# Kernel optimization log

Measured on AMD Instinct MI355X. Metric: run time of the kernel, lower is better.

## Reference

```python
import jax, jax.numpy as jnp
import numpy as np

BLOCK = 512
WINDOW = 2
NEG = -1e9


def _pad_to_block(x, block):
    pad_len = (-x.shape[1]) % block
    if pad_len:
        x = jnp.pad(x, ((0, 0), (0, pad_len), (0, 0)))
    return x


def setup_inputs() -> dict:
    key = jax.random.key(0)
    ks = jax.random.split(key, 8)
    B, Lq, Lk, C = 2, 8192, 8192, 128
    s = 1.0 / np.sqrt(C)
    return {
        "query": jax.random.normal(ks[0], (B, Lq, C), jnp.float32),
        "key_value": jax.random.normal(ks[1], (B, Lk, C), jnp.float32),
        "Wq": jax.random.normal(ks[2], (C, C), jnp.float32) * s,
        "bq": jax.random.normal(ks[3], (C,), jnp.float32) * 0.01,
        "Wkv": jax.random.normal(ks[4], (C, 2 * C), jnp.float32) * s,
        "bkv": jax.random.normal(ks[5], (2 * C,), jnp.float32) * 0.01,
        "Wo": jax.random.normal(ks[6], (C, C), jnp.float32) * s,
        "bo": jax.random.normal(ks[7], (C,), jnp.float32) * 0.01,
    }


def reference(query, key_value, Wq, bq, Wkv, bkv, Wo, bo):
    B, Lq, C = query.shape
    qp = _pad_to_block(query, BLOCK)
    kp = _pad_to_block(key_value, BLOCK)
    q = qp @ Wq + bq                      # [B, Lq_pad, C]
    kv = kp @ Wkv + bkv                   # [B, Lk_pad, 2C]
    k, v = kv[..., :C], kv[..., C:]
    nq = qp.shape[1] // BLOCK
    nk = kp.shape[1] // BLOCK
    qb = q.reshape(B, nq, BLOCK, C)
    kb = k.reshape(B, nk, BLOCK, C)
    vb = v.reshape(B, nk, BLOCK, C)
    allowed = jnp.abs(jnp.arange(nq)[:, None] - jnp.arange(nk)[None, :]) <= WINDOW  # [nq, nk]
    # scores: [B, nq, nk, s, d] with s = q-pos in block, d = k-pos in block
    scores = jnp.einsum('bqsc,bkdc->bqksd', qb, kb) / jnp.sqrt(jnp.asarray(C, qb.dtype))
    scores = jnp.where(allowed[None, :, :, None, None], scores, NEG)
    # NOTE: faithful to original torch code, softmax over axis=3 (the 's' axis)
    attn = jax.nn.softmax(scores, axis=3)
    out = jnp.einsum('bqksd,bkdc->bqsc', attn, vb)
    out = out.reshape(B, nq * BLOCK, C)[:, :Lq]
    return out @ Wo + bo
```

## Files before the change

### kernel.cpp

```cpp
#include <hip/hip_runtime.h>

typedef _Float16 f16;
typedef _Float16 half8 __attribute__((ext_vector_type(8)));
typedef float floatx4 __attribute__((ext_vector_type(4)));

#define MFMA16(a,b,c) __builtin_amdgcn_mfma_f32_16x16x32_f16((a),(b),(c),0,0,0)
#define RSL2E 0.12751743f

__device__ __forceinline__ void split2(float x, f16 &h, f16 &l) {
  f16 hh = (f16)x;
  h = hh;
  l = (f16)(x - (float)hh);
}

__device__ __forceinline__ void stage_rows64(const f16* __restrict__ g, int gstride,
                                             f16* lds, int rows, int tid, int nthr) {
  int total = rows * 8;
  for (int idx = tid; idx < total; idx += nthr) {
    int row = idx >> 3, slot = idx & 7;
    float4 v = *(const float4*)(g + (size_t)row * gstride + slot * 8);
    int lofs = ((row << 7) + (slot << 4)) ^ ((row & 7) << 4);
    *(float4*)((char*)lds + lofs) = v;
  }
}
__device__ __forceinline__ void stage_rows128(const f16* __restrict__ g, int gstride,
                                              f16* lds, int rows, int tid, int nthr) {
  int total = rows * 16;
  for (int idx = tid; idx < total; idx += nthr) {
    int row = idx >> 4, slot = idx & 15;
    float4 v = *(const float4*)(g + (size_t)row * gstride + slot * 8);
    int lofs = ((row << 8) + (slot << 4)) ^ ((row & 7) << 4);
    *(float4*)((char*)lds + lofs) = v;
  }
}
__device__ __forceinline__ void stage_split64(const float* __restrict__ g, int gstride,
                                              f16* ldsh, f16* ldsl, int rows,
                                              int tid, int nthr) {
  int total = rows * 16;
  for (int idx = tid; idx < total; idx += nthr) {
    int row = idx >> 4, cg = idx & 15;
    float4 va = *(const float4*)(g + (size_t)row * gstride + cg * 4);
    union { f16 a[4]; uint2 u; } hh, ll;
    split2(va.x, hh.a[0], ll.a[0]);
    split2(va.y, hh.a[1], ll.a[1]);
    split2(va.z, hh.a[2], ll.a[2]);
    split2(va.w, hh.a[3], ll.a[3]);
    int lofs = ((row << 7) + (cg << 3)) ^ ((row & 7) << 4);
    *(uint2*)((char*)ldsh + lofs) = hh.u;
    *(uint2*)((char*)ldsl + lofs) = ll.u;
  }
}
__device__ __forceinline__ half8 fragP128(const f16* lds, int row, int kofs) {
  int ofs = ((row << 7) + (kofs << 1)) ^ ((row & 7) << 4);
  return *(const half8*)((const char*)lds + ofs);
}
__device__ __forceinline__ half8 fragP256(const f16* lds, int row, int kofs) {
  int ofs = ((row << 8) + (kofs << 1)) ^ ((row & 7) << 4);
  return *(const half8*)((const char*)lds + ofs);
}

__global__ void k_splitW(const float* __restrict__ Wq, const float* __restrict__ Wkv,
                         const float* __restrict__ Wo,
                         f16* WqTh, f16* WqTl, f16* WkvTh, f16* WkvTl,
                         f16* WoTh, f16* WoTl) {
  int idx = blockIdx.x * 256 + threadIdx.x;
  if (idx >= 65536) return;
  float v; f16 *ph, *pl; int dst;
  if (idx < 16384) {
    int n = idx >> 7, c = idx & 127;
    v = Wq[c * 128 + n]; ph = WqTh; pl = WqTl; dst = idx;
  } else if (idx < 49152) {
    int t = idx - 16384; int n = t >> 7, c = t & 127;
    v = Wkv[c * 256 + n]; ph = WkvTh; pl = WkvTl; dst = t;
  } else {
    int t = idx - 49152; int n = t >> 7, c = t & 127;
    v = Wo[c * 128 + n]; ph = WoTh; pl = WoTl; dst = t;
  }
  f16 h, l; split2(v, h, l);
  ph[dst] = h; pl[dst] = l;
}

__global__ __launch_bounds__(512, 2)
void k_proj(const float* __restrict__ query, const float* __restrict__ key_value,
            const f16* __restrict__ WqTh, const f16* __restrict__ WqTl,
            const f16* __restrict__ WkvTh, const f16* __restrict__ WkvTl,
            const float* __restrict__ bq, const float* __restrict__ bkv,
            f16* __restrict__ qhp, f16* __restrict__ khp, f16* __restrict__ vT) {
  int pidx = blockIdx.x >> 8, blk = blockIdx.x & 255;
  const float* A; const f16 *BTh, *BTl; const float* bias; f16* out; int mode;
  if (pidx == 0)      { A = query;     BTh = WqTh;          BTl = WqTl;          bias = bq;        out = qhp; mode = 0; }
  else if (pidx == 1) { A = key_value; BTh = WkvTh;         BTl = WkvTl;         bias = bkv;       out = khp; mode = 0; }
  else                { A = key_value; BTh = WkvTh + 16384; BTl = WkvTl + 16384; bias = bkv + 128; out = vT;  mode = 1; }
  __shared__ f16 pool[24576];
  f16* sAh = pool;
  f16* sAl = pool + 4096;
  f16* sBh = pool + 8192;
  f16* sBl = pool + 16384;
  int tid = threadIdx.x, wave = tid >> 6, lane = tid & 63, lg = lane >> 4, lr = lane & 15;
  int wm = wave >> 2, wn = wave & 3;
  size_t rowbase = (size_t)blk * 64;
  floatx4 zero = {0.f, 0.f, 0.f, 0.f};
  floatx4 acc[2][2] = {{zero, zero}, {zero, zero}};
  for (int cc = 0; cc < 128; cc += 64) {
    __syncthreads();
    stage_split64(A + rowbase * 128 + cc, 128, sAh, sAl, 64, tid, 512);
    stage_rows64(BTh + cc, 128, sBh, 128, tid, 512);
    stage_rows64(BTl + cc, 128, sBl, 128, tid, 512);
    __syncthreads();
    for (int kc = 0; kc < 64; kc += 32) {
      half8 ah[2], al[2];
      for (int fm = 0; fm < 2; fm++) {
        ah[fm] = fragP128(sAh, wm * 32 + fm * 16 + lr, kc + lg * 8);
        al[fm] = fragP128(sAl, wm * 32 + fm * 16 + lr, kc + lg * 8);
      }
      for (int fn = 0; fn < 2; fn++) {
        half8 bh = fragP128(sBh, wn * 32 + fn * 16 + lr, kc + lg * 8);
        half8 bl = fragP128(sBl, wn * 32 + fn * 16 + lr, kc + lg * 8);
        for (int fm = 0; fm < 2; fm++) {
          acc[fm][fn] = MFMA16(ah[fm], bh, acc[fm][fn]);
          acc[fm][fn] = MFMA16(ah[fm], bl, acc[fm][fn]);
          acc[fm][fn] = MFMA16(al[fm], bh, acc[fm][fn]);
        }
      }
    }
  }
  __syncthreads();
  f16* e = pool;
  for (int fm = 0; fm < 2; fm++) for (int fn = 0; fn < 2; fn++) {
    int n = wn * 32 + fn * 16 + lr;
    float bs = bias[n];
    for (int jj = 0; jj < 4; jj++) {
      int m = wm * 32 + fm * 16 + lg * 4 + jj;
      e[m * 136 + n] = (f16)(acc[fm][fn][jj] + bs);
    }
  }
  __syncthreads();
  if (mode == 0) {
    for (int idx = tid; idx < 1024; idx += 512) {
      int r = idx >> 4, sl = idx & 15;
      *(float4*)(out + (rowbase + r) * 128 + sl * 8) =
          *(const float4*)((const char*)e + r * 272 + sl * 16);
    }
  } else {
    size_t bidx = rowbase >> 13, lofs = rowbase & 8191;
    for (int idx = tid; idx < 1024; idx += 512) {
      int c = idx >> 3, sl = idx & 7;
      union { f16 a[8]; float4 v; } th;
      for (int t = 0; t < 8; t++) th.a[t] = e[(sl * 8 + t) * 136 + c];
      *(float4*)(out + (bidx * 128 + c) * 8192 + lofs + sl * 8) = th.v;
    }
  }
}

__global__ __launch_bounds__(512, 2)
void k_final(const float* __restrict__ Pbuf, const float* __restrict__ U,
             const f16* __restrict__ BTh, const f16* __restrict__ BTl,
             const float* __restrict__ bias, float* __restrict__ out) {
  __shared__ f16 pool[24576];
  f16* sAh = pool;
  f16* sAl = pool + 4096;
  f16* sBh = pool + 8192;
  f16* sBl = pool + 16384;
  int tid = threadIdx.x, wave = tid >> 6, lane = tid & 63, lg = lane >> 4, lr = lane & 15;
  int wm = wave >> 2, wn = wave & 3;
  size_t rowbase = (size_t)blockIdx.x * 64;
  int b = (int)(rowbase >> 13), r0 = (int)(rowbase & 8191);
  int i = r0 >> 9, st = (r0 >> 6) & 7;
  const float* p0 = Pbuf + ((size_t)(((b * 16 + i) * 8 + st) * 4)) * 8192;
  const float* p1 = p0 + 8192;
  const float* p2 = p0 + 16384;
  const float* p3 = p0 + 24576;
  const float* Ub = U + ((size_t)b * 16 + i) * 128;
  floatx4 zero = {0.f, 0.f, 0.f, 0.f};
  floatx4 acc[2][2] = {{zero, zero}, {zero, zero}};
  for (int cc = 0; cc < 128; cc += 64) {
    __syncthreads();
    for (int idx = tid; idx < 1024; idx += 512) {
      int row = idx >> 4, cg = idx & 15;
      int c = cc + cg * 4;
      float4 a0 = *(const float4*)(p0 + row * 128 + c);
      float4 a1 = *(const float4*)(p1 + row * 128 + c);
      float4 a2 = *(const float4*)(p2 + row * 128 + c);
      float4 a3 = *(const float4*)(p3 + row * 128 + c);
      float4 uu = *(const float4*)(Ub + c);
      float vals[4] = {(a0.x + a1.x) + (a2.x + a3.x) + uu.x,
                       (a0.y + a1.y) + (a2.y + a3.y) + uu.y,
                       (a0.z + a1.z) + (a2.z + a3.z) + uu.z,
                       (a0.w + a1.w) + (a2.w + a3.w) + uu.w};
      union { f16 a[4]; uint2 u; } hh, ll;
      for (int t = 0; t < 4; t++) split2(vals[t], hh.a[t], ll.a[t]);
      int lofs = ((row << 7) + (cg << 3)) ^ ((row & 7) << 4);
      *(uint2*)((char*)sAh + lofs) = hh.u;
      *(uint2*)((char*)sAl + lofs) = ll.u;
    }
    stage_rows64(BTh + cc, 128, sBh, 128, tid, 512);
    stage_rows64(BTl + cc, 128, sBl, 128, tid, 512);
    __syncthreads();
    for (int kc = 0; kc < 64; kc += 32) {
      half8 ah[2], al[2];
      for (int fm = 0; fm < 2; fm++) {
        ah[fm] = fragP128(sAh, wm * 32 + fm * 16 + lr, kc + lg * 8);
        al[fm] = fragP128(sAl, wm * 32 + fm * 16 + lr, kc + lg * 8);
      }
      for (int fn = 0; fn < 2; fn++) {
        half8 bh = fragP128(sBh, wn * 32 + fn * 16 + lr, kc + lg * 8);
        half8 bl = fragP128(sBl, wn * 32 + fn * 16 + lr, kc + lg * 8);
        for (int fm = 0; fm < 2; fm++) {
          acc[fm][fn] = MFMA16(ah[fm], bh, acc[fm][fn]);
          acc[fm][fn] = MFMA16(ah[fm], bl, acc[fm][fn]);
          acc[fm][fn] = MFMA16(al[fm], bh, acc[fm][fn]);
        }
      }
    }
  }
  __syncthreads();
  float* ef = (float*)pool;
  for (int fm = 0; fm < 2; fm++) for (int fn = 0; fn < 2; fn++) {
    int n = wn * 32 + fn * 16 + lr;
    float bs = bias[n];
    for (int jj = 0; jj < 4; jj++) {
      int m = wm * 32 + fm * 16 + lg * 4 + jj;
      ef[m * 132 + n] = acc[fm][fn][jj] + bs;
    }
  }
  __syncthreads();
  for (int idx = tid; idx < 2048; idx += 512) {
    int r = idx >> 5, sl = idx & 31;
    *(float4*)(out + (rowbase + r) * 128 + sl * 4) = *(const float4*)(ef + r * 132 + sl * 4);
  }
}

__global__ void k_U(const f16* __restrict__ vT, float* __restrict__ U) {
  int b = blockIdx.x >> 7, c = blockIdx.x & 127;
  int tid = threadIdx.x;
  const f16* r = vT + ((size_t)b * 128 + c) * 8192;
  float s = 0.f;
  const float4* r4 = (const float4*)(r + tid * 32);
  for (int t = 0; t < 4; t++) {
    float4 v = r4[t];
    const f16* a = (const f16*)&v;
    for (int u = 0; u < 8; u++) s += (float)a[u];
  }
  __shared__ float part[256];
  __shared__ float bs[16];
  part[tid] = s;
  __syncthreads();
  if (tid < 16) {
    float t = 0.f;
    for (int u = 0; u < 16; u++) t += part[tid * 16 + u];
    bs[tid] = t;
  }
  __syncthreads();
  if (tid < 16) {
    int i = tid;
    float tot = 0.f;
    for (int j = 0; j < 16; j++) tot += bs[j];
    int j0 = i - 2 < 0 ? 0 : i - 2;
    int j1 = i + 2 > 15 ? 15 : i + 2;
    float win = 0.f;
    for (int j = j0; j <= j1; j++) win += bs[j];
    U[((size_t)b * 16 + i) * 128 + c] = (tot - win) * (1.0f / 512.0f);
  }
}

__global__ __launch_bounds__(512, 4)
void k_passA(const f16* __restrict__ kp, const f16* __restrict__ qp,
             float* __restrict__ Z) {
  int bid = blockIdx.x;
  int wg = (bid & 7) * 80 + (bid >> 3);
  int dchunk = wg & 3; int rest = wg >> 2;
  int slot = rest % 5; int rest2 = rest / 5;
  int i = rest2 & 15; int b = rest2 >> 4;
  int j = i - 2 + slot;
  if (j < 0 || j > 15) return;
  __shared__ f16 sK[16384], sQ[16384];
  int tid = threadIdx.x, wave = tid >> 6, lane = tid & 63, lg = lane >> 4, lr = lane & 15;
  int wm = wave >> 1, wn = wave & 1;
  size_t krow = (size_t)b * 8192 + j * 512 + dchunk * 128;
  stage_rows128(kp + krow * 128, 128, sK, 128, tid, 512);
  float zp[2][4] = {{0.f,0.f,0.f,0.f},{0.f,0.f,0.f,0.f}};
  floatx4 zero = {0.f, 0.f, 0.f, 0.f};
  for (int sc = 0; sc < 4; sc++) {
    __syncthreads();
    size_t qrow = (size_t)b * 8192 + i * 512 + sc * 128;
    stage_rows128(qp + qrow * 128, 128, sQ, 128, tid, 512);
    __syncthreads();
    floatx4 acc[2][4] = {{zero,zero,zero,zero},{zero,zero,zero,zero}};
    for (int kc = 0; kc < 128; kc += 32) {
      half8 ah[2];
      for (int fm = 0; fm < 2; fm++)
        ah[fm] = fragP256(sK, wm * 32 + fm * 16 + lr, kc + lg * 8);
      for (int fn = 0; fn < 4; fn++) {
        half8 bh = fragP256(sQ, wn * 64 + fn * 16 + lr, kc + lg * 8);
        for (int fm = 0; fm < 2; fm++)
          acc[fm][fn] = MFMA16(ah[fm], bh, acc[fm][fn]);
      }
    }
    for (int fm = 0; fm < 2; fm++) for (int fn = 0; fn < 4; fn++)
      for (int jj = 0; jj < 4; jj++)
        zp[fm][jj] += exp2f(acc[fm][fn][jj] * RSL2E);
  }
  for (int off = 1; off < 16; off <<= 1)
    for (int fm = 0; fm < 2; fm++) for (int jj = 0; jj < 4; jj++)
      zp[fm][jj] += __shfl_xor(zp[fm][jj], off, 64);
  __syncthreads();
  float* sred = (float*)sQ;
  if (lr == 0) {
    for (int fm = 0; fm < 2; fm++) for (int jj = 0; jj < 4; jj++) {
      int d = wm * 32 + fm * 16 + lg * 4 + jj;
      sred[wn * 128 + d] = zp[fm][jj];
    }
  }
  __syncthreads();
  if (tid < 128) {
    size_t zb = (((size_t)(b * 16 + i) * 16 + j) * 512) + dchunk * 128;
    Z[zb + tid] = sred[tid] + sred[128 + tid];
  }
}

__global__ __launch_bounds__(512, 4)
void k_passB(const f16* __restrict__ qp, const f16* __restrict__ kp,
             const f16* __restrict__ vT,
             const float* __restrict__ Z, float* __restrict__ Pbuf) {
  int bid = blockIdx.x;
  int wg = ((bid & 7) << 7) | (bid >> 3);
  int dq = wg & 3, st = (wg >> 2) & 7, i = (wg >> 5) & 15, b = wg >> 9;
  __shared__ __align__(16) char pool[40960];
  f16* sQ  = (f16*)pool;
  f16* sKV = (f16*)(pool + 16384);
  f16* sE  = (f16*)(pool + 32768);
  int tid = threadIdx.x, wave = tid >> 6, lane = tid & 63, lg = lane >> 4, lr = lane & 15;
  int w1m = wave >> 1, w1n = wave & 1;
  int w2m = wave >> 2, w2n = wave & 3;
  int krr = tid >> 3, ksl = tid & 7;
  int lofsA = ((krr << 7) + (ksl << 4)) ^ ((krr & 7) << 4);
  int lofsB = (((krr + 64) << 7) + (ksl << 4)) ^ ((krr & 7) << 4);
  size_t qrow = (size_t)b * 8192 + i * 512 + st * 64;
  stage_rows128(qp + qrow * 128, 128, sQ, 64, tid, 512);
  floatx4 zero = {0.f, 0.f, 0.f, 0.f};
  floatx4 acc2[2][2] = {{zero, zero}, {zero, zero}};
  for (int slot = 0; slot < 5; slot++) {
    int j = i - 2 + slot;
    if (j < 0 || j > 15) continue;
    {
      int dchunk = dq;
      const f16* kb = kp + ((size_t)b * 8192 + j * 512 + dchunk * 128) * 128;
      float4 p0a = *(const float4*)(kb + krr * 128 + ksl * 8);
      float4 p0b = *(const float4*)(kb + (krr + 64) * 128 + ksl * 8);
      floatx4 acc1[2][2] = {{zero, zero}, {zero, zero}};
      __syncthreads();
      *(float4*)((char*)sKV + lofsA) = p0a;
      *(float4*)((char*)sKV + lofsB) = p0b;
      float4 p1a = *(const float4*)(kb + krr * 128 + 64 + ksl * 8);
      float4 p1b = *(const float4*)(kb + (krr + 64) * 128 + 64 + ksl * 8);
      __syncthreads();
      for (int kc = 0; kc < 64; kc += 32) {
        half8 ah[2];
        for (int fm = 0; fm < 2; fm++)
          ah[fm] = fragP128(sKV, w1m * 32 + fm * 16 + lr, kc + lg * 8);
        for (int fn = 0; fn < 2; fn++) {
          half8 bh = fragP256(sQ, w1n * 32 + fn * 16 + lr, kc + lg * 8);
          for (int fm = 0; fm < 2; fm++)
            acc1[fm][fn] = MFMA16(ah[fm], bh, acc1[fm][fn]);
        }
      }
      __syncthreads();
      *(float4*)((char*)sKV + lofsA) = p1a;
      *(float4*)((char*)sKV + lofsB) = p1b;
      __syncthreads();
      for (int kc = 0; kc < 64; kc += 32) {
        half8 ah[2];
        for (int fm = 0; fm < 2; fm++)
          ah[fm] = fragP128(sKV, w1m * 32 + fm * 16 + lr, kc + lg * 8);
        for (int fn = 0; fn < 2; fn++) {
          half8 bh = fragP256(sQ, w1n * 32 + fn * 16 + lr, 64 + kc + lg * 8);
          for (int fm = 0; fm < 2; fm++)
            acc1[fm][fn] = MFMA16(ah[fm], bh, acc1[fm][fn]);
        }
      }
      float rz[2][4];
      {
        size_t zb = (((size_t)(b * 16 + i) * 16 + j) * 512) + dchunk * 128;
        for (int fm = 0; fm < 2; fm++) for (int jj = 0; jj < 4; jj++)
          rz[fm][jj] = 1.0f / Z[zb + w1m * 32 + fm * 16 + lg * 4 + jj];
      }
      for (int dsub = 0; dsub < 2; dsub++) {
        __syncthreads();
        if ((w1m >> 1) == dsub) {
          for (int fm = 0; fm < 2; fm++) for (int fn = 0; fn < 2; fn++)
            for (int jj = 0; jj < 4; jj++) {
              int dl = w1m * 32 + fm * 16 + lg * 4 + jj;
              int ds = dl - dsub * 64;
              int s = w1n * 32 + fn * 16 + lr;
              float e = exp2f(acc1[fm][fn][jj] * RSL2E) * rz[fm][jj];
              int ofs = ((s << 7) + (ds << 1)) ^ ((s & 7) << 4);
              *(f16*)((char*)sE + ofs) = (f16)e;
            }
        } else {
          int tt = (wave >= 4) ? (tid - 256) : tid;
          size_t vcol = (size_t)j * 512 + dchunk * 128 + dsub * 64;
          const f16* gv = vT + (size_t)b * 128 * 8192 + vcol;
          for (int idx = tt; idx < 1024; idx += 256) {
            int row = idx >> 3, sl = idx & 7;
            int lofs = ((row << 7) + (sl << 4)) ^ ((row & 7) << 4);
            *(float4*)((char*)sKV + lofs) = *(const float4*)(gv + (size_t)row * 8192 + sl * 8);
          }
        }
        __syncthreads();
        for (int kc = 0; kc < 64; kc += 32) {
          half8 ah[2];
          for (int fm = 0; fm < 2; fm++)
            ah[fm] = fragP128(sE, w2m * 32 + fm * 16 + lr, kc + lg * 8);
          for (int fn = 0; fn < 2; fn++) {
            half8 bh = fragP128(sKV, w2n * 32 + fn * 16 + lr, kc + lg * 8);
            for (int fm = 0; fm < 2; fm++)
              acc2[fm][fn] = MFMA16(ah[fm], bh, acc2[fm][fn]);
          }
        }
      }
    }
  }
  __syncthreads();
  float* ef = (float*)pool;
  for (int fm = 0; fm < 2; fm++) for (int fn = 0; fn < 2; fn++) {
    int c = w2n * 32 + fn * 16 + lr;
    for (int jj = 0; jj < 4; jj++) {
      int s = w2m * 32 + fm * 16 + lg * 4 + jj;
      ef[s * 128 + c] = acc2[fm][fn][jj];
    }
  }
  __syncthreads();
  float* po = Pbuf + ((size_t)((((b * 16 + i) * 8 + st) * 4) + dq)) * 8192;
  for (int idx = tid; idx < 2048; idx += 512)
    ((float4*)po)[idx] = ((const float4*)ef)[idx];
}

extern "C" void kernel_launch(void* const* d_in, const int* in_sizes, int n_in,
                              void* d_out, int out_size, void* d_ws, size_t ws_size,
                              hipStream_t stream) {
  const float* query     = (const float*)d_in[0];
  const float* key_value = (const float*)d_in[1];
  const float* Wq  = (const float*)d_in[2];
  const float* bq  = (const float*)d_in[3];
  const float* Wkv = (const float*)d_in[4];
  const float* bkv = (const float*)d_in[5];
  const float* Wo  = (const float*)d_in[6];
  const float* bo  = (const float*)d_in[7];
  float* out = (float*)d_out;

  char* ws = (char*)d_ws;
  size_t off = 0;
  auto alloc = [&](size_t bytes) -> char* {
    char* p = ws + off;
    off += (bytes + 255) & ~(size_t)255;
    return p;
  };
  const size_t SZH = (size_t)16384 * 128 * 2;
  f16* qhp  = (f16*)alloc(SZH);
  f16* khp  = (f16*)alloc(SZH);
  f16* vT   = (f16*)alloc(SZH);
  float* Pbuf = (float*)alloc((size_t)1024 * 8192 * 4);
  f16* WqTh  = (f16*)alloc(32768); f16* WqTl  = (f16*)alloc(32768);
  f16* WkvTh = (f16*)alloc(65536); f16* WkvTl = (f16*)alloc(65536);
  f16* WoTh  = (f16*)alloc(32768); f16* WoTl  = (f16*)alloc(32768);
  float* Zb = (float*)alloc((size_t)2 * 16 * 16 * 512 * 4);
  float* Ub = (float*)alloc((size_t)2 * 16 * 128 * 4);
  if (off > ws_size) return;

  k_splitW<<<256, 256, 0, stream>>>(Wq, Wkv, Wo, WqTh, WqTl, WkvTh, WkvTl, WoTh, WoTl);
  k_proj<<<768, 512, 0, stream>>>(query, key_value, WqTh, WqTl, WkvTh, WkvTl,
                                  bq, bkv, qhp, khp, vT);
  k_U<<<256, 256, 0, stream>>>(vT, Ub);
  k_passA<<<640, 512, 0, stream>>>(khp, qhp, Zb);
  k_passB<<<1024, 512, 0, stream>>>(qhp, khp, vT, Zb, Pbuf);
  k_final<<<256, 512, 0, stream>>>(Pbuf, Ub, WoTh, WoTl, bo, out);
}
```

Measured before the change: 126.7 us.

## Prefetch V tiles and Z reciprocals into registers before QK MFMA phase

Global loads of the V^T tile and the Z normalizers move to the start of each key-block iteration, held in registers, so their latency overlaps the score MFMAs instead of stalling the exp/PV phase. The exp results are packed four f16 at a time into a single 8-byte LDS store instead of scalar half stores. Which wave group writes exponents versus stages V is now selected by wave index. This adds about 16 extra live VGPRs per thread under launch_bounds(512,4), which risks spilling or lower occupancy.

```diff
diff --git a/kernel.cpp b/kernel.cpp
--- a/kernel.cpp
+++ b/kernel.cpp
@@ -335,10 +335,18 @@
   int krr = tid >> 3, ksl = tid & 7;
   int lofsA = ((krr << 7) + (ksl << 4)) ^ ((krr & 7) << 4);
   int lofsB = (((krr + 64) << 7) + (ksl << 4)) ^ ((krr & 7) << 4);
+  int myVdsub = (wave < 4) ? 1 : 0;
+  int tt = (wave >= 4) ? (tid - 256) : tid;
+  int vr0 = tt >> 3, vsl = tt & 7;
+  int vlofs[4];
+  #pragma unroll
+  for (int t = 0; t < 4; t++)
+    vlofs[t] = (((vr0 + 32 * t) << 7) + (vsl << 4)) ^ ((vr0 & 7) << 4);
   size_t qrow = (size_t)b * 8192 + i * 512 + st * 64;
   stage_rows128(qp + qrow * 128, 128, sQ, 64, tid, 512);
   floatx4 zero = {0.f, 0.f, 0.f, 0.f};
   floatx4 acc2[2][2] = {{zero, zero}, {zero, zero}};
+  const f16* vbase = vT + (size_t)b * 1048576;
   for (int slot = 0; slot < 5; slot++) {
     int j = i - 2 + slot;
     if (j < 0 || j > 15) continue;
@@ -347,6 +355,20 @@
       const f16* kb = kp + ((size_t)b * 8192 + j * 512 + dchunk * 128) * 128;
       float4 p0a = *(const float4*)(kb + krr * 128 + ksl * 8);
       float4 p0b = *(const float4*)(kb + (krr + 64) * 128 + ksl * 8);
+      const f16* gv = vbase + (size_t)j * 512 + dchunk * 128 + myVdsub * 64;
+      float4 vr_0 = *(const float4*)(gv + (size_t)vr0 * 8192 + vsl * 8);
+      float4 vr_1 = *(const float4*)(gv + (size_t)(vr0 + 32) * 8192 + vsl * 8);
+      float4 vr_2 = *(const float4*)(gv + (size_t)(vr0 + 64) * 8192 + vsl * 8);
+      float4 vr_3 = *(const float4*)(gv + (size_t)(vr0 + 96) * 8192 + vsl * 8);
+      float rz[2][4];
+      {
+        size_t zb = (((size_t)(b * 16 + i) * 16 + j) * 512) + dchunk * 128;
+        #pragma unroll
+        for (int fm = 0; fm < 2; fm++)
+          #pragma unroll
+          for (int jj = 0; jj < 4; jj++)
+            rz[fm][jj] = 1.0f / Z[zb + w1m * 32 + fm * 16 + lg * 4 + jj];
+      }
       floatx4 acc1[2][2] = {{zero, zero}, {zero, zero}};
       __syncthreads();
       *(float4*)((char*)sKV + lofsA) = p0a;
@@ -378,33 +400,27 @@
             acc1[fm][fn] = MFMA16(ah[fm], bh, acc1[fm][fn]);
         }
       }
-      float rz[2][4];
-      {
-        size_t zb = (((size_t)(b * 16 + i) * 16 + j) * 512) + dchunk * 128;
-        for (int fm = 0; fm < 2; fm++) for (int jj = 0; jj < 4; jj++)
-          rz[fm][jj] = 1.0f / Z[zb + w1m * 32 + fm * 16 + lg * 4 + jj];
-      }
       for (int dsub = 0; dsub < 2; dsub++) {
         __syncthreads();
-        if ((w1m >> 1) == dsub) {
-          for (int fm = 0; fm < 2; fm++) for (int fn = 0; fn < 2; fn++)
-            for (int jj = 0; jj < 4; jj++) {
-              int dl = w1m * 32 + fm * 16 + lg * 4 + jj;
-              int ds = dl - dsub * 64;
+        if ((wave >> 2) == dsub) {
+          #pragma unroll
+          for (int fm = 0; fm < 2; fm++)
+            #pragma unroll
+            for (int fn = 0; fn < 2; fn++) {
               int s = w1n * 32 + fn * 16 + lr;
-              float e = exp2f(acc1[fm][fn][jj] * RSL2E) * rz[fm][jj];
-              int ofs = ((s << 7) + (ds << 1)) ^ ((s & 7) << 4);
-              *(f16*)((char*)sE + ofs) = (f16)e;
+              int ds0 = (w1m & 1) * 32 + fm * 16 + lg * 4;
+              union { f16 a[4]; float2 u; } pk;
+              #pragma unroll
+              for (int jj = 0; jj < 4; jj++)
+                pk.a[jj] = (f16)(exp2f(acc1[fm][fn][jj] * RSL2E) * rz[fm][jj]);
+              int ofs = ((s << 7) + (ds0 << 1)) ^ ((s & 7) << 4);
+              *(float2*)((char*)sE + ofs) = pk.u;
             }
         } else {
-          int tt = (wave >= 4) ? (tid - 256) : tid;
-          size_t vcol = (size_t)j * 512 + dchunk * 128 + dsub * 64;
-          const f16* gv = vT + (size_t)b * 128 * 8192 + vcol;
-          for (int idx = tt; idx < 1024; idx += 256) {
-            int row = idx >> 3, sl = idx & 7;
-            int lofs = ((row << 7) + (sl << 4)) ^ ((row & 7) << 4);
-            *(float4*)((char*)sKV + lofs) = *(const float4*)(gv + (size_t)row * 8192 + sl * 8);
-          }
+          *(float4*)((char*)sKV + vlofs[0]) = vr_0;
+          *(float4*)((char*)sKV + vlofs[1]) = vr_1;
+          *(float4*)((char*)sKV + vlofs[2]) = vr_2;
+          *(float4*)((char*)sKV + vlofs[3]) = vr_3;
         }
         __syncthreads();
         for (int kc = 0; kc < 64; kc += 32) {
```

Result: faster. 113.4 us (-10.5%).
